# Optimization experiments

Hardware: AMD Instinct MI355X
Metric: run time of the kernel (lower is better)

Reference implementation:

```python
import jax, jax.numpy as jnp
import numpy as np

B, S, D = 4, 2048, 1024


def setup_inputs() -> dict:
    key = jax.random.key(0)
    ks = jax.random.split(key, 7)
    s = 1.0 / np.sqrt(D)
    return {
        "x": jax.random.normal(ks[0], (B, S, D), dtype=jnp.float32),
        "Wq": jax.random.normal(ks[1], (D, D), dtype=jnp.float32) * s,
        "bq": jax.random.normal(ks[2], (D,), dtype=jnp.float32) * 0.01,
        "Wk": jax.random.normal(ks[3], (D, D), dtype=jnp.float32) * s,
        "bk": jax.random.normal(ks[4], (D,), dtype=jnp.float32) * 0.01,
        "Wv": jax.random.normal(ks[5], (D, D), dtype=jnp.float32) * s,
        "bv": jax.random.normal(ks[6], (D,), dtype=jnp.float32) * 0.01,
    }


def reference(x, Wq, bq, Wk, bk, Wv, bv):
    # x: [B, S, D]; Linear uses y = x @ W^T + b (torch convention)
    q = jnp.einsum("bsd,ed->bse", x, Wq) + bq
    k = jnp.einsum("bsd,ed->bse", x, Wk) + bk
    v = jnp.einsum("bsd,ed->bse", x, Wv) + bv
    # NOTE: original module applies softmax(q k^T) with NO 1/sqrt(d) scaling
    scores = jnp.einsum("bqd,bkd->bqk", q, k)  # [B, S, S]
    attn = jax.nn.softmax(scores, axis=-1)
    return jnp.einsum("bqk,bkd->bqd", attn, v)  # [B, S, D]
```

## Files before the change

### kernel.cpp

```cpp
#include <hip/hip_runtime.h>


#define Bb 4
#define Ss 2048
#define Dd 1024
#define Mtot 8192

typedef _Float16 f16x8 __attribute__((ext_vector_type(8)));
typedef float f32x4 __attribute__((ext_vector_type(4)));
typedef int i32x4 __attribute__((ext_vector_type(4)));
typedef signed char i8x16 __attribute__((ext_vector_type(16)));
typedef unsigned short u16;
typedef unsigned int u32;
typedef unsigned char u8;
typedef u16 u16x8 __attribute__((ext_vector_type(8)));
typedef u16 u16x4 __attribute__((ext_vector_type(4)));
typedef void __attribute__((address_space(1))) gvoid_t;
typedef void __attribute__((address_space(3))) svoid_t;

#define XC 0.0625f
#define XCI 16.f
#define XFI 4096.f
#define WC 1.953125e-3f
#define WCI 512.f
#define WFI 131072.f
#define W1S 7.62939453125e-6f
#define SM_P 1.220703125e-4f
#define SX_P 4.76837158203125e-7f
#define SY_P 1.862645149230957e-9f
#define SG00 3.814697265625e-6f
#define SG01 1.4901161193847656e-8f
#define SG11 5.820766091346741e-11f

__device__ __forceinline__ void gl_lds16(const void* g, void* l) {
  __builtin_amdgcn_global_load_lds((gvoid_t*)g, (svoid_t*)l, 16, 0, 0);
}

__device__ __forceinline__ u16 f2h(float f) {
  return __builtin_bit_cast(u16, (_Float16)f);
}
__device__ __forceinline__ f16x8 frag_ld_h(const char* p) {
  u16x8 v = *(const u16x8*)p;
  return __builtin_bit_cast(f16x8, v);
}
__device__ __forceinline__ f32x4 mfma_f16(f16x8 a, f16x8 b, f32x4 c) {
  return __builtin_amdgcn_mfma_f32_16x16x32_f16(a, b, c, 0, 0, 0);
}
__device__ __forceinline__ i32x4 mfma_i8(i32x4 a, i32x4 b, i32x4 c) {
  return __builtin_amdgcn_mfma_i32_16x16x64_i8(a, b, c, 0, 0, 0);
}
__device__ __forceinline__ void dig2(float v, float cs, float ci, float fi,
                                     int& d0, int& d1) {
  float t = fminf(fmaxf(v * ci, -127.f), 127.f);
  d0 = __float2int_rn(t);
  float res = v - (float)d0 * cs;
  float u = fminf(fmaxf(res * fi, -127.f), 127.f);
  d1 = __float2int_rn(u);
}

template <int GX, int GY, int GZ>
__device__ __forceinline__ void xcd_swz(int& bx, int& by, int& bz) {
  constexpr int N = GX * GY * GZ;
  int flat = (int)blockIdx.x + GX * ((int)blockIdx.y + GY * (int)blockIdx.z);
  int s = (flat & 7) * (N >> 3) + (flat >> 3);
  bx = s & (GX - 1);
  by = (s / GX) & (GY - 1);
  bz = s / (GX * GY);
}

__device__ __forceinline__ void wait_bar_keep8() {
  asm volatile("s_waitcnt vmcnt(8)" ::: "memory");
  __builtin_amdgcn_s_barrier();
  __builtin_amdgcn_sched_barrier(0);
}
__device__ __forceinline__ void wait_bar_drain() {
  asm volatile("s_waitcnt vmcnt(0)" ::: "memory");
  __builtin_amdgcn_s_barrier();
  __builtin_amdgcn_sched_barrier(0);
}
__device__ __forceinline__ void end_bar() {
  __builtin_amdgcn_sched_barrier(0);
  __builtin_amdgcn_s_barrier();
}

template <int ROUNDS, int C>
__device__ __forceinline__ void stageF(const char* g, long row0, long ldb,
                                       long k0b, char* l, int tid) {
#pragma unroll
  for (int r = 0; r < ROUNDS; ++r) {
    int s = r * 256 + tid;
    int sub = s / (16 * C);
    int t = s % (16 * C);
    int h = t >> 6;
    int lk = (t >> 4) & 3;
    int lr = t & 15;
    gl_lds16(g + (row0 + sub * 16 + lr) * ldb + k0b + (h * 4 + lk) * 16,
             l + s * 16);
  }
}

__global__ void __launch_bounds__(256) convert_w(
    const float* __restrict__ Wq, const float* __restrict__ Wk,
    const float* __restrict__ Wv,
    u8* __restrict__ wq0, u8* __restrict__ wq1,
    u8* __restrict__ wk0, u8* __restrict__ wk1, u16* __restrict__ wvh) {
  long b = blockIdx.x;
  if (b < 2048) {
    int which = (int)(b >> 10);
    const float* src = which ? Wk : Wq;
    u8* o0 = which ? wk0 : wq0;
    u8* o1 = which ? wk1 : wq1;
    long i = (b & 1023) * 256 + threadIdx.x;
    f32x4 v = ((const f32x4*)src)[i];
    u32 p0 = 0, p1 = 0;
#pragma unroll
    for (int j = 0; j < 4; ++j) {
      int d0, d1;
      dig2(v[j], WC, WCI, WFI, d0, d1);
      p0 |= ((u32)(d0 & 255)) << (8 * j);
      p1 |= ((u32)(d1 & 255)) << (8 * j);
    }
    ((u32*)o0)[i] = p0;
    ((u32*)o1)[i] = p1;
  } else {
    long i = (b - 2048) * 256 + threadIdx.x;
    f32x4 v = ((const f32x4*)Wv)[i];
    u16x4 h;
#pragma unroll
    for (int j = 0; j < 4; ++j) h[j] = f2h(v[j]);
    ((u16x4*)wvh)[i] = h;
  }
}

__global__ void __launch_bounds__(256) transpose_w(
    const u8* __restrict__ wq0, const u8* __restrict__ wq1,
    const u8* __restrict__ wk0, const u8* __restrict__ wk1,
    u8* __restrict__ wqT0, u8* __restrict__ wqT1,
    u8* __restrict__ wkT0, u8* __restrict__ wkT1) {
  __shared__ u8 T[64][68];
  int a = blockIdx.z;
  const u8* src = a == 0 ? wq0 : a == 1 ? wq1 : a == 2 ? wk0 : wk1;
  u8* dst = a == 0 ? wqT0 : a == 1 ? wqT1 : a == 2 ? wkT0 : wkT1;
  int bi = blockIdx.y, bj = blockIdx.x;
  int t = threadIdx.x, r = t >> 2, c4 = t & 3;
  const u32* s = (const u32*)(src + (long)(bi * 64 + r) * 1024 + bj * 64 + c4 * 16);
  u32 v0 = s[0], v1 = s[1], v2 = s[2], v3 = s[3];
  u32* trow = (u32*)&T[r][c4 * 16];
  trow[0] = v0; trow[1] = v1; trow[2] = v2; trow[3] = v3;
  __syncthreads();
  u32 o[4] = {0, 0, 0, 0};
#pragma unroll
  for (int j = 0; j < 16; ++j)
    o[j >> 2] |= ((u32)T[c4 * 16 + j][r]) << (8 * (j & 3));
  u32* d = (u32*)(dst + (long)(bj * 64 + r) * 1024 + bi * 64 + c4 * 16);
  d[0] = o[0]; d[1] = o[1]; d[2] = o[2]; d[3] = o[3];
}

__global__ void __launch_bounds__(256) gvec_kernel(
    const u8* __restrict__ wqT0, const u8* __restrict__ wqT1,
    const u8* __restrict__ wkT0, const u8* __restrict__ wkT1,
    const float* __restrict__ bq, const float* __restrict__ bk,
    float* __restrict__ gq, float* __restrict__ gk, float* __restrict__ cbuf) {
  __shared__ float sbq[1024], sbk[1024];
  int tid = threadIdx.x;
  ((f32x4*)sbq)[tid] = ((const f32x4*)bq)[tid];
  ((f32x4*)sbk)[tid] = ((const f32x4*)bk)[tid];
  __syncthreads();
  int wave = tid >> 6, lane = tid & 63;
#pragma unroll
  for (int rr = 0; rr < 2; ++rr) {
    int d = blockIdx.x * 8 + wave * 2 + rr;
    i8x16 a0 = *(const i8x16*)(wqT0 + (long)d * 1024 + lane * 16);
    i8x16 a1 = *(const i8x16*)(wqT1 + (long)d * 1024 + lane * 16);
    i8x16 c0 = *(const i8x16*)(wkT0 + (long)d * 1024 + lane * 16);
    i8x16 c1 = *(const i8x16*)(wkT1 + (long)d * 1024 + lane * 16);
    float sq = 0.f, sk = 0.f;
#pragma unroll
    for (int j = 0; j < 16; ++j) {
      sq += ((float)a0[j] * WC + (float)a1[j] * W1S) * sbk[lane * 16 + j];
      sk += ((float)c0[j] * WC + (float)c1[j] * W1S) * sbq[lane * 16 + j];
    }
#pragma unroll
    for (int off = 32; off >= 1; off >>= 1) {
      sq += __shfl_xor(sq, off);
      sk += __shfl_xor(sk, off);
    }
    if (!lane) { gq[d] = sq; gk[d] = sk; }
  }
  if (blockIdx.x == 0 && wave == 0) {
    float c = 0.f;
#pragma unroll
    for (int j = 0; j < 16; ++j) c += sbq[lane * 16 + j] * sbk[lane * 16 + j];
#pragma unroll
    for (int off = 32; off >= 1; off >>= 1) c += __shfl_xor(c, off);
    if (!lane) cbuf[0] = c;
  }
}

__global__ void __launch_bounds__(256) convert_x(
    const float* __restrict__ x, const float* __restrict__ gq,
    const float* __restrict__ gk, const float* __restrict__ cbuf,
    u16* __restrict__ xh, u8* __restrict__ xd0, u8* __restrict__ xd1,
    float* __restrict__ ubuf, float* __restrict__ wbuf) {
  long b = blockIdx.x;
  int tid = threadIdx.x;
  long i = b * 256 + tid;
  f32x4 v = ((const f32x4*)x)[i];
  u16x4 h;
  u32 p0 = 0, p1 = 0;
#pragma unroll
  for (int j = 0; j < 4; ++j) {
    h[j] = f2h(v[j]);
    int d0, d1;
    dig2(v[j], XC, XCI, XFI, d0, d1);
    p0 |= ((u32)(d0 & 255)) << (8 * j);
    p1 |= ((u32)(d1 & 255)) << (8 * j);
  }
  ((u16x4*)xh)[i] = h;
  ((u32*)xd0)[i] = p0;
  ((u32*)xd1)[i] = p1;

  f32x4 g4 = ((const f32x4*)gq)[tid];
  f32x4 k4 = ((const f32x4*)gk)[tid];
  float pu = v[0] * g4[0] + v[1] * g4[1] + v[2] * g4[2] + v[3] * g4[3];
  float pw = v[0] * k4[0] + v[1] * k4[1] + v[2] * k4[2] + v[3] * k4[3];
#pragma unroll
  for (int off = 32; off >= 1; off >>= 1) {
    pu += __shfl_xor(pu, off);
    pw += __shfl_xor(pw, off);
  }
  __shared__ float ru[4], rw[4];
  int wave = tid >> 6, lane = tid & 63;
  if (!lane) { ru[wave] = pu; rw[wave] = pw; }
  __syncthreads();
  if (!tid) {
    ubuf[b] = ru[0] + ru[1] + ru[2] + ru[3] + cbuf[0];
    wbuf[b] = rw[0] + rw[1] + rw[2] + rw[3];
  }
}

__global__ void __launch_bounds__(256, 2) g_part(
    const u8* __restrict__ wqT0, const u8* __restrict__ wqT1,
    const u8* __restrict__ wkT0, const u8* __restrict__ wkT1,
    float* __restrict__ Gpart) {
  __shared__ char lds[65536];
  const int tid = threadIdx.x;
  const int bx = blockIdx.x, by = blockIdx.y, bz = blockIdx.z;
  const long m0 = (long)by * 128;
  const int n0 = bx * 128;
  const int k00 = bz * 256;
  const int wave = tid >> 6, lane = tid & 63;
  const int wm = wave >> 1, wn = wave & 1;
  const int lr = lane & 15, lk = lane >> 4;

  i32x4 accM[4][4] = {};
  i32x4 accX[4][4] = {};
  i32x4 accY[4][4] = {};

  auto stage = [&](char* L, int kk) {
    stageF<2, 4>((const char*)wqT0, m0, 1024, kk, L + 0, tid);
    stageF<2, 4>((const char*)wqT1, m0, 1024, kk, L + 8192, tid);
    stageF<2, 4>((const char*)wkT0, n0, 1024, kk, L + 16384, tid);
    stageF<2, 4>((const char*)wkT1, n0, 1024, kk, L + 24576, tid);
  };
  auto compute = [&](const char* L) {
    i32x4 b0[4], b1[4];
#pragma unroll
    for (int nt = 0; nt < 4; ++nt) {
      int rb = (wn * 4 + nt) * 1024 + lane * 16;
      b0[nt] = *(const i32x4*)(L + 16384 + rb);
      b1[nt] = *(const i32x4*)(L + 24576 + rb);
    }
    __builtin_amdgcn_s_setprio(1);
#pragma unroll
    for (int mt = 0; mt < 4; ++mt) {
      int ra = (wm * 4 + mt) * 1024 + lane * 16;
      i32x4 a0 = *(const i32x4*)(L + ra);
      i32x4 a1 = *(const i32x4*)(L + 8192 + ra);
#pragma unroll
      for (int nt = 0; nt < 4; ++nt) {
        accM[mt][nt] = mfma_i8(a0, b0[nt], accM[mt][nt]);
        accX[mt][nt] = mfma_i8(a0, b1[nt], accX[mt][nt]);
        accX[mt][nt] = mfma_i8(a1, b0[nt], accX[mt][nt]);
        accY[mt][nt] = mfma_i8(a1, b1[nt], accY[mt][nt]);
      }
    }
    __builtin_amdgcn_s_setprio(0);
  };

  stage(lds, k00);
  for (int t = 0; t < 3; ++t) {
    char* L = lds + (t & 1) * 32768;
    stage(lds + ((t + 1) & 1) * 32768, k00 + (t + 1) * 64);
    wait_bar_keep8();
    compute(L);
    end_bar();
  }
  {
    char* L = lds + 32768;
    wait_bar_drain();
    compute(L);
  }

#pragma unroll
  for (int mt = 0; mt < 4; ++mt)
#pragma unroll
    for (int nt = 0; nt < 4; ++nt) {
      int e = n0 + wn * 64 + nt * 16 + lr;
      int gmb = (int)m0 + wm * 64 + mt * 16 + lk * 4;
      f32x4 o;
#pragma unroll
      for (int r = 0; r < 4; ++r)
        o[r] = (float)accM[mt][nt][r] * SG00 + (float)accX[mt][nt][r] * SG01 +
               (float)accY[mt][nt][r] * SG11;
      *(f32x4*)(Gpart + ((long)bz << 20) + (long)e * 1024 + gmb) = o;
    }
}

__global__ void __launch_bounds__(256) g_reduce(const float* __restrict__ Gpart,
                                                u8* __restrict__ Gt0,
                                                u8* __restrict__ Gt1) {
  int n = blockIdx.x, tid = threadIdx.x;
  long o = (long)n * 1024 + tid * 4;
  f32x4 v = *(const f32x4*)(Gpart + o);
  f32x4 v1 = *(const f32x4*)(Gpart + (1L << 20) + o);
  f32x4 v2 = *(const f32x4*)(Gpart + (2L << 20) + o);
  f32x4 v3 = *(const f32x4*)(Gpart + (3L << 20) + o);
#pragma unroll
  for (int j = 0; j < 4; ++j) v[j] = v[j] + v1[j] + v2[j] + v3[j];
  u32 p0 = 0, p1 = 0;
#pragma unroll
  for (int j = 0; j < 4; ++j) {
    int d0, d1;
    dig2(v[j], WC, WCI, WFI, d0, d1);
    p0 |= ((u32)(d0 & 255)) << (8 * j);
    p1 |= ((u32)(d1 & 255)) << (8 * j);
  }
  ((u32*)Gt0)[n * 256 + tid] = p0;
  ((u32*)Gt1)[n * 256 + tid] = p1;
}

__global__ void __launch_bounds__(256, 2) t_gemm(
    const u8* __restrict__ xd0, const u8* __restrict__ xd1,
    const u8* __restrict__ Gt0, const u8* __restrict__ Gt1,
    u16* __restrict__ th) {
  __shared__ char lds[65536];
  const int tid = threadIdx.x;
  int bx, by, bz;
  xcd_swz<8, 64, 1>(bx, by, bz);
  const long m0 = (long)by * 128;
  const int n0 = bx * 128;
  const int wave = tid >> 6, lane = tid & 63;
  const int wm = wave >> 1, wn = wave & 1;
  const int lr = lane & 15, lk = lane >> 4;

  i32x4 accM[4][4] = {};
  i32x4 accX[4][4] = {};
  i32x4 accY[4][4] = {};

  auto stage = [&](char* L, int kk) {
    stageF<2, 4>((const char*)xd0, m0, Dd, kk, L + 0, tid);
    stageF<2, 4>((const char*)xd1, m0, Dd, kk, L + 8192, tid);
    stageF<2, 4>((const char*)Gt0, n0, 1024, kk, L + 16384, tid);
    stageF<2, 4>((const char*)Gt1, n0, 1024, kk, L + 24576, tid);
  };
  auto compute = [&](const char* L) {
    i32x4 b0[4], b1[4];
#pragma unroll
    for (int nt = 0; nt < 4; ++nt) {
      int rb = (wn * 4 + nt) * 1024 + lane * 16;
      b0[nt] = *(const i32x4*)(L + 16384 + rb);
      b1[nt] = *(const i32x4*)(L + 24576 + rb);
    }
    __builtin_amdgcn_s_setprio(1);
#pragma unroll
    for (int mt = 0; mt < 4; ++mt) {
      int ra = (wm * 4 + mt) * 1024 + lane * 16;
      i32x4 a0 = *(const i32x4*)(L + ra);
      i32x4 a1 = *(const i32x4*)(L + 8192 + ra);
#pragma unroll
      for (int nt = 0; nt < 4; ++nt) {
        accM[mt][nt] = mfma_i8(a0, b0[nt], accM[mt][nt]);
        accX[mt][nt] = mfma_i8(a0, b1[nt], accX[mt][nt]);
        accX[mt][nt] = mfma_i8(a1, b0[nt], accX[mt][nt]);
        accY[mt][nt] = mfma_i8(a1, b1[nt], accY[mt][nt]);
      }
    }
    __builtin_amdgcn_s_setprio(0);
  };

  stage(lds, 0);
  for (int t = 0; t < Dd / 64 - 1; ++t) {
    char* L = lds + (t & 1) * 32768;
    stage(lds + ((t + 1) & 1) * 32768, (t + 1) * 64);
    wait_bar_keep8();
    compute(L);
    end_bar();
  }
  {
    char* L = lds + ((Dd / 64 - 1) & 1) * 32768;
    wait_bar_drain();
    compute(L);
  }

#pragma unroll
  for (int mt = 0; mt < 4; ++mt)
#pragma unroll
    for (int nt = 0; nt < 4; ++nt)
#pragma unroll
      for (int r = 0; r < 4; ++r) {
        long gm = m0 + wm * 64 + mt * 16 + lk * 4 + r;
        int e = n0 + wn * 64 + nt * 16 + lr;
        float v = (float)accM[mt][nt][r] * SM_P +
                  (float)accX[mt][nt][r] * SX_P +
                  (float)accY[mt][nt][r] * SY_P;
        th[gm * Dd + e] = f2h(v);
      }
}

__global__ void __launch_bounds__(256) v_gemm(
    const u16* __restrict__ xh, const u16* __restrict__ wvh,
    const float* __restrict__ bv, u16* __restrict__ vt) {
  __shared__ char lds[65536];
  const int tid = threadIdx.x;
  int bx, by, bz;
  xcd_swz<8, 64, 1>(bx, by, bz);
  const long m0 = (long)by * 128;
  const int n0 = bx * 128;
  const int wave = tid >> 6, lane = tid & 63;
  const int wm = wave >> 1, wn = wave & 1;
  const int lr = lane & 15, lk = lane >> 4;

  f32x4 acc[4][4] = {};

  auto stage = [&](char* L, int k0) {
    stageF<4, 8>((const char*)xh, m0, (long)Dd * 2, (long)k0 * 2, L + 0, tid);
    stageF<4, 8>((const char*)wvh, n0, (long)Dd * 2, (long)k0 * 2, L + 16384, tid);
  };
  auto compute = [&](const char* L) {
    f16x8 af[2][4], bfr[2][4];
#pragma unroll
    for (int ks = 0; ks < 2; ++ks)
#pragma unroll
      for (int i = 0; i < 4; ++i) {
        af[ks][i] = frag_ld_h(L + (wm * 4 + i) * 2048 + ks * 1024 + lane * 16);
        bfr[ks][i] = frag_ld_h(L + 16384 + (wn * 4 + i) * 2048 + ks * 1024 + lane * 16);
      }
    __builtin_amdgcn_s_setprio(1);
#pragma unroll
    for (int ks = 0; ks < 2; ++ks)
#pragma unroll
      for (int mt = 0; mt < 4; ++mt)
#pragma unroll
        for (int nt = 0; nt < 4; ++nt)
          acc[mt][nt] = mfma_f16(af[ks][mt], bfr[ks][nt], acc[mt][nt]);
    __builtin_amdgcn_s_setprio(0);
  };

  stage(lds, 0);
  for (int t = 0; t < Dd / 64 - 1; ++t) {
    char* L = lds + (t & 1) * 32768;
    stage(lds + ((t + 1) & 1) * 32768, (t + 1) * 64);
    wait_bar_keep8();
    compute(L);
    end_bar();
  }
  {
    char* L = lds + ((Dd / 64 - 1) & 1) * 32768;
    wait_bar_drain();
    compute(L);
  }

#pragma unroll
  for (int mt = 0; mt < 4; ++mt)
#pragma unroll
    for (int nt = 0; nt < 4; ++nt)
#pragma unroll
      for (int r = 0; r < 4; ++r) {
        long gm = m0 + wm * 64 + mt * 16 + lk * 4 + r;
        int e = n0 + wn * 64 + nt * 16 + lr;
        float v = acc[mt][nt][r] + bv[e];
        long b = gm >> 11, s = gm & 2047;
        vt[(b * Dd + e) * (long)Ss + s] = f2h(v);
      }
}

__global__ void __launch_bounds__(256, 2) score_gemm(
    const u16* __restrict__ th, const u16* __restrict__ xh,
    const float* __restrict__ ubuf, const float* __restrict__ wbuf,
    float* __restrict__ scores) {
  __shared__ char lds[65536];
  const int tid = threadIdx.x;
  int bx, by, bz;
  xcd_swz<16, 16, 4>(bx, by, bz);
  const int z = bz;
  const long base = (long)z * Ss * Dd * 2;
  const long m0 = (long)by * 128;
  const int n0 = bx * 128;
  const int wave = tid >> 6, lane = tid & 63;
  const int wm = wave >> 1, wn = wave & 1;
  const int lr = lane & 15, lk = lane >> 4;

  f32x4 acc[4][4] = {};

  auto stage = [&](char* L, int k0) {
    stageF<4, 8>((const char*)th + base, m0, (long)Dd * 2, (long)k0 * 2, L + 0, tid);
    stageF<4, 8>((const char*)xh + base, n0, (long)Dd * 2, (long)k0 * 2, L + 16384, tid);
  };
  auto compute = [&](const char* L) {
    f16x8 af[2][4], bfr[2][4];
#pragma unroll
    for (int ks = 0; ks < 2; ++ks)
#pragma unroll
      for (int i = 0; i < 4; ++i) {
        af[ks][i] = frag_ld_h(L + (wm * 4 + i) * 2048 + ks * 1024 + lane * 16);
        bfr[ks][i] = frag_ld_h(L + 16384 + (wn * 4 + i) * 2048 + ks * 1024 + lane * 16);
      }
    __builtin_amdgcn_s_setprio(1);
#pragma unroll
    for (int ks = 0; ks < 2; ++ks)
#pragma unroll
      for (int mt = 0; mt < 4; ++mt)
#pragma unroll
        for (int nt = 0; nt < 4; ++nt)
          acc[mt][nt] = mfma_f16(af[ks][mt], bfr[ks][nt], acc[mt][nt]);
    __builtin_amdgcn_s_setprio(0);
  };

  stage(lds, 0);
  for (int t = 0; t < Dd / 64 - 1; ++t) {
    char* L = lds + (t & 1) * 32768;
    stage(lds + ((t + 1) & 1) * 32768, (t + 1) * 64);
    wait_bar_keep8();
    compute(L);
    end_bar();
  }
  {
    char* L = lds + ((Dd / 64 - 1) & 1) * 32768;
    wait_bar_drain();
    compute(L);
  }

  float* srow = scores + (long)z * Ss * Ss;
#pragma unroll
  for (int mt = 0; mt < 4; ++mt)
#pragma unroll
    for (int nt = 0; nt < 4; ++nt)
#pragma unroll
      for (int r = 0; r < 4; ++r) {
        long i = m0 + wm * 64 + mt * 16 + lk * 4 + r;
        int j = n0 + wn * 64 + nt * 16 + lr;
        srow[i * Ss + j] = acc[mt][nt][r] +
                           ubuf[(z << 11) + i] + wbuf[(z << 11) + j];
      }
}

__global__ void __launch_bounds__(256) softmax_rows(const float* __restrict__ scores,
                                                    u16* __restrict__ P) {
  const long r = blockIdx.x;
  const float* row = scores + r * Ss;
  u16* prow = P + r * Ss;
  const int t = threadIdx.x;
  const int wave = t >> 6, lane = t & 63;
  f32x4 v0 = ((const f32x4*)row)[t * 2];
  f32x4 v1 = ((const f32x4*)row)[t * 2 + 1];
  float a[8];
#pragma unroll
  for (int j = 0; j < 4; ++j) { a[j] = v0[j]; a[4 + j] = v1[j]; }

  float m = a[0];
#pragma unroll
  for (int j = 1; j < 8; ++j) m = fmaxf(m, a[j]);
#pragma unroll
  for (int off = 32; off >= 1; off >>= 1) m = fmaxf(m, __shfl_xor(m, off));
  __shared__ float red[4];
  if (lane == 0) red[wave] = m;
  __syncthreads();
  m = fmaxf(fmaxf(red[0], red[1]), fmaxf(red[2], red[3]));

  float e[8];
  float s = 0.f;
#pragma unroll
  for (int j = 0; j < 8; ++j) { e[j] = __expf(a[j] - m); s += e[j]; }
#pragma unroll
  for (int off = 32; off >= 1; off >>= 1) s += __shfl_xor(s, off);
  __syncthreads();
  if (lane == 0) red[wave] = s;
  __syncthreads();
  s = red[0] + red[1] + red[2] + red[3];
  float inv = 1.0f / s;

  u16x8 pk;
#pragma unroll
  for (int j = 0; j < 8; ++j) pk[j] = f2h(e[j] * inv);
  ((u16x8*)prow)[t] = pk;
}

__global__ void __launch_bounds__(256) pv_gemm(const u16* __restrict__ P,
                                               const u16* __restrict__ vt,
                                               float* __restrict__ out) {
  __shared__ char lds[65536];
  const int tid = threadIdx.x;
  int bx, by, bz;
  xcd_swz<8, 16, 4>(bx, by, bz);
  const int z = bz;
  const u16* A = P + (long)z * Ss * Ss;
  const u16* Bp = vt + (long)z * Dd * Ss;
  const long m0 = (long)by * 128;
  const int n0 = bx * 128;

  const int wave = tid >> 6, lane = tid & 63;
  const int wm = wave >> 1, wn = wave & 1;
  const int lr = lane & 15, lk = lane >> 4;

  f32x4 acc[4][4] = {};

  auto stage = [&](char* L, int k0) {
    stageF<4, 8>((const char*)A, m0, (long)Ss * 2, (long)k0 * 2, L + 0, tid);
    stageF<4, 8>((const char*)Bp, n0, (long)Ss * 2, (long)k0 * 2, L + 16384, tid);
  };
  auto compute = [&](const char* L) {
    f16x8 af[2][4], bfr[2][4];
#pragma unroll
    for (int ks = 0; ks < 2; ++ks)
#pragma unroll
      for (int i = 0; i < 4; ++i) {
        af[ks][i] = frag_ld_h(L + (wm * 4 + i) * 2048 + ks * 1024 + lane * 16);
        bfr[ks][i] = frag_ld_h(L + 16384 + (wn * 4 + i) * 2048 + ks * 1024 + lane * 16);
      }
    __builtin_amdgcn_s_setprio(1);
#pragma unroll
    for (int ks = 0; ks < 2; ++ks)
#pragma unroll
      for (int mt = 0; mt < 4; ++mt)
#pragma unroll
        for (int nt = 0; nt < 4; ++nt)
          acc[mt][nt] = mfma_f16(af[ks][mt], bfr[ks][nt], acc[mt][nt]);
    __builtin_amdgcn_s_setprio(0);
  };

  stage(lds, 0);
  for (int t = 0; t < Ss / 64 - 1; ++t) {
    char* L = lds + (t & 1) * 32768;
    stage(lds + ((t + 1) & 1) * 32768, (t + 1) * 64);
    wait_bar_keep8();
    compute(L);
    end_bar();
  }
  {
    char* L = lds + ((Ss / 64 - 1) & 1) * 32768;
    wait_bar_drain();
    compute(L);
  }

  float* orow = out + (long)z * Ss * Dd;
#pragma unroll
  for (int mt = 0; mt < 4; ++mt)
#pragma unroll
    for (int nt = 0; nt < 4; ++nt)
#pragma unroll
      for (int r = 0; r < 4; ++r) {
        long i = m0 + wm * 64 + mt * 16 + lk * 4 + r;
        int e = n0 + wn * 64 + nt * 16 + lr;
        orow[i * Dd + e] = acc[mt][nt][r];
      }
}

extern "C" void kernel_launch(void* const* d_in, const int* in_sizes, int n_in,
                              void* d_out, int out_size, void* d_ws, size_t ws_size,
                              hipStream_t stream) {
  const float* x = (const float*)d_in[0];
  const float* Wq = (const float*)d_in[1];
  const float* bq = (const float*)d_in[2];
  const float* Wk = (const float*)d_in[3];
  const float* bk = (const float*)d_in[4];
  const float* Wv = (const float*)d_in[5];
  const float* bv = (const float*)d_in[6];
  float* out = (float*)d_out;

  char* p = (char*)d_ws;
  float* scores = (float*)p;
  u8* Gt0 = (u8*)p;
  u8* Gt1 = (u8*)(p + (1L << 20));
  u16* wvh = (u16*)(p + (16L << 20));
  u8* xd0 = (u8*)(p + (64L << 20));
  u8* xd1 = (u8*)(p + (72L << 20));
  u16* th = (u16*)(p + (80L << 20));
  u8* wq0 = (u8*)(p + (80L << 20));
  u8* wq1 = wq0 + (1L << 20);
  u8* wk0 = wq0 + (2L << 20);
  u8* wk1 = wq0 + (3L << 20);
  float* Gpart = (float*)(p + (80L << 20));
  u16* Pbuf = (u16*)(p + (96L << 20));
  u16* xh = (u16*)(p + (96L << 20));
  u16* vt = (u16*)(p + (128L << 20));
  u8* wqT0 = (u8*)(p + (144L << 20));
  u8* wqT1 = wqT0 + (1L << 20);
  u8* wkT0 = wqT0 + (2L << 20);
  u8* wkT1 = wqT0 + (3L << 20);
  float* gq = (float*)(p + (148L << 20));
  float* gk = gq + 1024;
  float* ubuf = gq + 2048;
  float* wbuf = ubuf + 8192;
  float* cbuf = wbuf + 8192;

  convert_w<<<dim3(3072), dim3(256), 0, stream>>>(Wq, Wk, Wv, wq0, wq1, wk0, wk1, wvh);
  transpose_w<<<dim3(16, 16, 4), dim3(256), 0, stream>>>(
      wq0, wq1, wk0, wk1, wqT0, wqT1, wkT0, wkT1);
  gvec_kernel<<<dim3(128), dim3(256), 0, stream>>>(
      wqT0, wqT1, wkT0, wkT1, bq, bk, gq, gk, cbuf);
  convert_x<<<dim3(8192), dim3(256), 0, stream>>>(
      x, gq, gk, cbuf, xh, xd0, xd1, ubuf, wbuf);
  v_gemm<<<dim3(Dd / 128, Mtot / 128), dim3(256), 0, stream>>>(xh, wvh, bv, vt);
  g_part<<<dim3(8, 8, 4), dim3(256), 0, stream>>>(wqT0, wqT1, wkT0, wkT1, Gpart);
  g_reduce<<<dim3(1024), dim3(256), 0, stream>>>(Gpart, Gt0, Gt1);
  t_gemm<<<dim3(Dd / 128, Mtot / 128), dim3(256), 0, stream>>>(
      xd0, xd1, Gt0, Gt1, th);
  score_gemm<<<dim3(Ss / 128, Ss / 128, Bb), dim3(256), 0, stream>>>(
      th, xh, ubuf, wbuf, scores);
  softmax_rows<<<dim3(Bb * Ss), dim3(256), 0, stream>>>(scores, Pbuf);
  pv_gemm<<<dim3(Dd / 128, Ss / 128, Bb), dim3(256), 0, stream>>>(Pbuf, vt, out);
}
```

Before: 352.2 us.

## Replace split-int8 t_gemm with single fp16 MFMA GEMM, shrink score_gemm K-tile

The t_gemm projection (x times the folded Wq^T Wk matrix G) previously split both operands into two int8 digits and ran four i8 MFMAs per tile. It now uses the fp16 copy of x and an fp16 G produced by g_reduce, which drops the digit packing in convert_x and g_reduce and cuts the MFMA work in t_gemm. Separately, score_gemm moves to a 32-wide K step with half the LDS and a launch bound of 4 blocks per CU to raise occupancy. The trade-off is lower precision in th, since the G entries and the accumulated products lose the extra int8 digit.

```diff
diff --git a/kernel.cpp b/kernel.cpp
--- a/kernel.cpp
+++ b/kernel.cpp
@@ -18,16 +18,10 @@
 typedef void __attribute__((address_space(1))) gvoid_t;
 typedef void __attribute__((address_space(3))) svoid_t;
 
-#define XC 0.0625f
-#define XCI 16.f
-#define XFI 4096.f
 #define WC 1.953125e-3f
 #define WCI 512.f
 #define WFI 131072.f
 #define W1S 7.62939453125e-6f
-#define SM_P 1.220703125e-4f
-#define SX_P 4.76837158203125e-7f
-#define SY_P 1.862645149230957e-9f
 #define SG00 3.814697265625e-6f
 #define SG01 1.4901161193847656e-8f
 #define SG11 5.820766091346741e-11f
@@ -70,6 +64,11 @@
 
 __device__ __forceinline__ void wait_bar_keep8() {
   asm volatile("s_waitcnt vmcnt(8)" ::: "memory");
+  __builtin_amdgcn_s_barrier();
+  __builtin_amdgcn_sched_barrier(0);
+}
+__device__ __forceinline__ void wait_bar_keep4() {
+  asm volatile("s_waitcnt vmcnt(4)" ::: "memory");
   __builtin_amdgcn_s_barrier();
   __builtin_amdgcn_sched_barrier(0);
 }
@@ -200,25 +199,15 @@
 __global__ void __launch_bounds__(256) convert_x(
     const float* __restrict__ x, const float* __restrict__ gq,
     const float* __restrict__ gk, const float* __restrict__ cbuf,
-    u16* __restrict__ xh, u8* __restrict__ xd0, u8* __restrict__ xd1,
-    float* __restrict__ ubuf, float* __restrict__ wbuf) {
+    u16* __restrict__ xh, float* __restrict__ ubuf, float* __restrict__ wbuf) {
   long b = blockIdx.x;
   int tid = threadIdx.x;
   long i = b * 256 + tid;
   f32x4 v = ((const f32x4*)x)[i];
   u16x4 h;
-  u32 p0 = 0, p1 = 0;
-#pragma unroll
-  for (int j = 0; j < 4; ++j) {
-    h[j] = f2h(v[j]);
-    int d0, d1;
-    dig2(v[j], XC, XCI, XFI, d0, d1);
-    p0 |= ((u32)(d0 & 255)) << (8 * j);
-    p1 |= ((u32)(d1 & 255)) << (8 * j);
-  }
+#pragma unroll
+  for (int j = 0; j < 4; ++j) h[j] = f2h(v[j]);
   ((u16x4*)xh)[i] = h;
-  ((u32*)xd0)[i] = p0;
-  ((u32*)xd1)[i] = p1;
 
   f32x4 g4 = ((const f32x4*)gq)[tid];
   f32x4 k4 = ((const f32x4*)gk)[tid];
@@ -318,31 +307,21 @@
 }
 
 __global__ void __launch_bounds__(256) g_reduce(const float* __restrict__ Gpart,
-                                                u8* __restrict__ Gt0,
-                                                u8* __restrict__ Gt1) {
+                                                u16* __restrict__ Gh) {
   int n = blockIdx.x, tid = threadIdx.x;
   long o = (long)n * 1024 + tid * 4;
   f32x4 v = *(const f32x4*)(Gpart + o);
   f32x4 v1 = *(const f32x4*)(Gpart + (1L << 20) + o);
   f32x4 v2 = *(const f32x4*)(Gpart + (2L << 20) + o);
   f32x4 v3 = *(const f32x4*)(Gpart + (3L << 20) + o);
-#pragma unroll
-  for (int j = 0; j < 4; ++j) v[j] = v[j] + v1[j] + v2[j] + v3[j];
-  u32 p0 = 0, p1 = 0;
-#pragma unroll
-  for (int j = 0; j < 4; ++j) {
-    int d0, d1;
-    dig2(v[j], WC, WCI, WFI, d0, d1);
-    p0 |= ((u32)(d0 & 255)) << (8 * j);
-    p1 |= ((u32)(d1 & 255)) << (8 * j);
-  }
-  ((u32*)Gt0)[n * 256 + tid] = p0;
-  ((u32*)Gt1)[n * 256 + tid] = p1;
-}
-
-__global__ void __launch_bounds__(256, 2) t_gemm(
-    const u8* __restrict__ xd0, const u8* __restrict__ xd1,
-    const u8* __restrict__ Gt0, const u8* __restrict__ Gt1,
+  u16x4 h;
+#pragma unroll
+  for (int j = 0; j < 4; ++j) h[j] = f2h(v[j] + v1[j] + v2[j] + v3[j]);
+  ((u16x4*)Gh)[n * 256 + tid] = h;
+}
+
+__global__ void __launch_bounds__(256) t_gemm(
+    const u16* __restrict__ xh, const u16* __restrict__ Gh,
     u16* __restrict__ th) {
   __shared__ char lds[65536];
   const int tid = threadIdx.x;
@@ -354,38 +333,29 @@
   const int wm = wave >> 1, wn = wave & 1;
   const int lr = lane & 15, lk = lane >> 4;
 
-  i32x4 accM[4][4] = {};
-  i32x4 accX[4][4] = {};
-  i32x4 accY[4][4] = {};
-
-  auto stage = [&](char* L, int kk) {
-    stageF<2, 4>((const char*)xd0, m0, Dd, kk, L + 0, tid);
-    stageF<2, 4>((const char*)xd1, m0, Dd, kk, L + 8192, tid);
-    stageF<2, 4>((const char*)Gt0, n0, 1024, kk, L + 16384, tid);
-    stageF<2, 4>((const char*)Gt1, n0, 1024, kk, L + 24576, tid);
+  f32x4 acc[4][4] = {};
+
+  auto stage = [&](char* L, int k0) {
+    stageF<4, 8>((const char*)xh, m0, (long)Dd * 2, (long)k0 * 2, L + 0, tid);
+    stageF<4, 8>((const char*)Gh, n0, (long)Dd * 2, (long)k0 * 2, L + 16384, tid);
   };
   auto compute = [&](const char* L) {
-    i32x4 b0[4], b1[4];
-#pragma unroll
-    for (int nt = 0; nt < 4; ++nt) {
-      int rb = (wn * 4 + nt) * 1024 + lane * 16;
-      b0[nt] = *(const i32x4*)(L + 16384 + rb);
-      b1[nt] = *(const i32x4*)(L + 24576 + rb);
-    }
+    f16x8 af[2][4], bfr[2][4];
+#pragma unroll
+    for (int ks = 0; ks < 2; ++ks)
+#pragma unroll
+      for (int i = 0; i < 4; ++i) {
+        af[ks][i] = frag_ld_h(L + (wm * 4 + i) * 2048 + ks * 1024 + lane * 16);
+        bfr[ks][i] = frag_ld_h(L + 16384 + (wn * 4 + i) * 2048 + ks * 1024 + lane * 16);
+      }
     __builtin_amdgcn_s_setprio(1);
 #pragma unroll
-    for (int mt = 0; mt < 4; ++mt) {
-      int ra = (wm * 4 + mt) * 1024 + lane * 16;
-      i32x4 a0 = *(const i32x4*)(L + ra);
-      i32x4 a1 = *(const i32x4*)(L + 8192 + ra);
-#pragma unroll
-      for (int nt = 0; nt < 4; ++nt) {
-        accM[mt][nt] = mfma_i8(a0, b0[nt], accM[mt][nt]);
-        accX[mt][nt] = mfma_i8(a0, b1[nt], accX[mt][nt]);
-        accX[mt][nt] = mfma_i8(a1, b0[nt], accX[mt][nt]);
-        accY[mt][nt] = mfma_i8(a1, b1[nt], accY[mt][nt]);
-      }
-    }
+    for (int ks = 0; ks < 2; ++ks)
+#pragma unroll
+      for (int mt = 0; mt < 4; ++mt)
+#pragma unroll
+        for (int nt = 0; nt < 4; ++nt)
+          acc[mt][nt] = mfma_f16(af[ks][mt], bfr[ks][nt], acc[mt][nt]);
     __builtin_amdgcn_s_setprio(0);
   };
 
@@ -411,10 +381,7 @@
       for (int r = 0; r < 4; ++r) {
         long gm = m0 + wm * 64 + mt * 16 + lk * 4 + r;
         int e = n0 + wn * 64 + nt * 16 + lr;
-        float v = (float)accM[mt][nt][r] * SM_P +
-                  (float)accX[mt][nt][r] * SX_P +
-                  (float)accY[mt][nt][r] * SY_P;
-        th[gm * Dd + e] = f2h(v);
+        th[gm * Dd + e] = f2h(acc[mt][nt][r]);
       }
 }
 
@@ -485,11 +452,11 @@
       }
 }
 
-__global__ void __launch_bounds__(256, 2) score_gemm(
+__global__ void __launch_bounds__(256, 4) score_gemm(
     const u16* __restrict__ th, const u16* __restrict__ xh,
     const float* __restrict__ ubuf, const float* __restrict__ wbuf,
     float* __restrict__ scores) {
-  __shared__ char lds[65536];
+  __shared__ char lds[32768];
   const int tid = threadIdx.x;
   int bx, by, bz;
   xcd_swz<16, 16, 4>(bx, by, bz);
@@ -504,39 +471,35 @@
   f32x4 acc[4][4] = {};
 
   auto stage = [&](char* L, int k0) {
-    stageF<4, 8>((const char*)th + base, m0, (long)Dd * 2, (long)k0 * 2, L + 0, tid);
-    stageF<4, 8>((const char*)xh + base, n0, (long)Dd * 2, (long)k0 * 2, L + 16384, tid);
+    stageF<2, 4>((const char*)th + base, m0, (long)Dd * 2, (long)k0 * 2, L + 0, tid);
+    stageF<2, 4>((const char*)xh + base, n0, (long)Dd * 2, (long)k0 * 2, L + 8192, tid);
   };
   auto compute = [&](const char* L) {
-    f16x8 af[2][4], bfr[2][4];
-#pragma unroll
-    for (int ks = 0; ks < 2; ++ks)
-#pragma unroll
-      for (int i = 0; i < 4; ++i) {
-        af[ks][i] = frag_ld_h(L + (wm * 4 + i) * 2048 + ks * 1024 + lane * 16);
-        bfr[ks][i] = frag_ld_h(L + 16384 + (wn * 4 + i) * 2048 + ks * 1024 + lane * 16);
-      }
+    f16x8 af[4], bfr[4];
+#pragma unroll
+    for (int i = 0; i < 4; ++i) {
+      af[i] = frag_ld_h(L + (wm * 4 + i) * 1024 + lane * 16);
+      bfr[i] = frag_ld_h(L + 8192 + (wn * 4 + i) * 1024 + lane * 16);
+    }
     __builtin_amdgcn_s_setprio(1);
 #pragma unroll
-    for (int ks = 0; ks < 2; ++ks)
-#pragma unroll
-      for (int mt = 0; mt < 4; ++mt)
-#pragma unroll
-        for (int nt = 0; nt < 4; ++nt)
-          acc[mt][nt] = mfma_f16(af[ks][mt], bfr[ks][nt], acc[mt][nt]);
+    for (int mt = 0; mt < 4; ++mt)
+#pragma unroll
+      for (int nt = 0; nt < 4; ++nt)
+        acc[mt][nt] = mfma_f16(af[mt], bfr[nt], acc[mt][nt]);
     __builtin_amdgcn_s_setprio(0);
   };
 
   stage(lds, 0);
-  for (int t = 0; t < Dd / 64 - 1; ++t) {
-    char* L = lds + (t & 1) * 32768;
-    stage(lds + ((t + 1) & 1) * 32768, (t + 1) * 64);
-    wait_bar_keep8();
+  for (int t = 0; t < Dd / 32 - 1; ++t) {
+    char* L = lds + (t & 1) * 16384;
+    stage(lds + ((t + 1) & 1) * 16384, (t + 1) * 32);
+    wait_bar_keep4();
     compute(L);
     end_bar();
   }
   {
-    char* L = lds + ((Dd / 64 - 1) & 1) * 32768;
+    char* L = lds + ((Dd / 32 - 1) & 1) * 16384;
     wait_bar_drain();
     compute(L);
   }
@@ -680,11 +643,8 @@
 
   char* p = (char*)d_ws;
   float* scores = (float*)p;
-  u8* Gt0 = (u8*)p;
-  u8* Gt1 = (u8*)(p + (1L << 20));
+  u16* Gh = (u16*)p;
   u16* wvh = (u16*)(p + (16L << 20));
-  u8* xd0 = (u8*)(p + (64L << 20));
-  u8* xd1 = (u8*)(p + (72L << 20));
   u16* th = (u16*)(p + (80L << 20));
   u8* wq0 = (u8*)(p + (80L << 20));
   u8* wq1 = wq0 + (1L << 20);
@@ -710,12 +670,11 @@
   gvec_kernel<<<dim3(128), dim3(256), 0, stream>>>(
       wqT0, wqT1, wkT0, wkT1, bq, bk, gq, gk, cbuf);
   convert_x<<<dim3(8192), dim3(256), 0, stream>>>(
-      x, gq, gk, cbuf, xh, xd0, xd1, ubuf, wbuf);
+      x, gq, gk, cbuf, xh, ubuf, wbuf);
   v_gemm<<<dim3(Dd / 128, Mtot / 128), dim3(256), 0, stream>>>(xh, wvh, bv, vt);
   g_part<<<dim3(8, 8, 4), dim3(256), 0, stream>>>(wqT0, wqT1, wkT0, wkT1, Gpart);
-  g_reduce<<<dim3(1024), dim3(256), 0, stream>>>(Gpart, Gt0, Gt1);
-  t_gemm<<<dim3(Dd / 128, Mtot / 128), dim3(256), 0, stream>>>(
-      xd0, xd1, Gt0, Gt1, th);
+  g_reduce<<<dim3(1024), dim3(256), 0, stream>>>(Gpart, Gh);
+  t_gemm<<<dim3(Dd / 128, Mtot / 128), dim3(256), 0, stream>>>(xh, Gh, th);
   score_gemm<<<dim3(Ss / 128, Ss / 128, Bb), dim3(256), 0, stream>>>(
       th, xh, ubuf, wbuf, scores);
   softmax_rows<<<dim3(Bb * Ss), dim3(256), 0, stream>>>(scores, Pbuf);
```

Measured after the change: 348.4 us. Within noise of the previous version (-1.1%).
